# Kernel optimization log

Measured on AMD Instinct MI355X. Metric: run time of the kernel, lower is better.

## Reference

```python
import jax, jax.numpy as jnp
import numpy as np

N_NODES = 200000
N_EDGES = 500000
N_RELS = 256
D = 256  # rnn_in_dim == rnn_hid_dim


def setup_inputs() -> dict:
    key = jax.random.key(0)
    ks = jax.random.split(key, 8)
    src_nid = jax.random.randint(ks[0], (N_EDGES,), 0, N_NODES, dtype=jnp.int32)
    dst_nid = jax.random.randint(ks[1], (N_EDGES,), 0, N_NODES, dtype=jnp.int32)
    rel = jax.random.randint(ks[2], (N_EDGES,), 0, N_RELS, dtype=jnp.int32)
    static_entity_emb = jax.random.normal(ks[3], (N_NODES, D), dtype=jnp.float32)
    dynamic_relation_emb = jax.random.normal(ks[4], (N_RELS, 1, D, 2), dtype=jnp.float32)
    s = 1.0 / np.sqrt(D)
    W_ih = jax.random.uniform(ks[5], (3 * D, D), jnp.float32, -s, s)
    W_hh = jax.random.uniform(ks[6], (3 * D, D), jnp.float32, -s, s)
    kb1, kb2 = jax.random.split(ks[7])
    b_ih = jax.random.uniform(kb1, (3 * D,), jnp.float32, -s, s)
    b_hh = jax.random.uniform(kb2, (3 * D,), jnp.float32, -s, s)
    return {"src_nid": src_nid, "dst_nid": dst_nid, "rel": rel,
            "static_entity_emb": static_entity_emb,
            "dynamic_relation_emb": dynamic_relation_emb,
            "W_ih": W_ih, "W_hh": W_hh, "b_ih": b_ih, "b_hh": b_hh}


def _segment_mean(x, ids, num_segments):
    # x: [E, D], ids: [E] -> [R, D] mean per relation (0 where empty, as scatter_mean)
    sums = jax.ops.segment_sum(x, ids, num_segments=num_segments)
    cnts = jax.ops.segment_sum(jnp.ones((ids.shape[0],), x.dtype), ids,
                               num_segments=num_segments)
    return sums / jnp.maximum(cnts, 1.0)[:, None]


def _gru_cell(x, h, W_ih, W_hh, b_ih, b_hh):
    # PyTorch GRU cell, single step. x,h: [R, H]
    gi = x @ W_ih.T + b_ih            # [R, 3H]
    gh = h @ W_hh.T + b_hh            # [R, 3H]
    i_r, i_z, i_n = jnp.split(gi, 3, axis=-1)
    h_r, h_z, h_n = jnp.split(gh, 3, axis=-1)
    r = jax.nn.sigmoid(i_r + h_r)
    z = jax.nn.sigmoid(i_z + h_z)
    n = jnp.tanh(i_n + r * h_n)
    return (1.0 - z) * n + z * h


def reference(src_nid, dst_nid, rel, static_entity_emb, dynamic_relation_emb,
              W_ih, W_hh, b_ih, b_hh):
    R = dynamic_relation_emb.shape[0]
    # gather node embeddings by edge endpoints, mean-reduce per relation
    src_avg = _segment_mean(static_entity_emb[src_nid], rel, R)  # [R, D]
    dst_avg = _segment_mean(static_entity_emb[dst_nid], rel, R)  # [R, D]
    h_src = dynamic_relation_emb[:, 0, :, 0]  # num_layers==1 -> [R, H]
    h_dst = dynamic_relation_emb[:, 0, :, 1]
    new_src = _gru_cell(src_avg, h_src, W_ih, W_hh, b_ih, b_hh)
    new_dst = _gru_cell(dst_avg, h_dst, W_ih, W_hh, b_ih, b_hh)
    # [R, num_layers=1, H, 2]
    return jnp.stack([new_src, new_dst], axis=-1)[:, None, :, :]
```

## Files before the change

kernel.cpp:

```cpp
#include <hip/hip_runtime.h>
#include <math.h>

#define D 256
#define R 256
#define DIMC 64

__device__ __forceinline__ float sigmoidf(float x) {
    return 1.0f / (1.0f + expf(-x));
}

__global__ void zero_ws(float* ws, int n) {
    int i = blockIdx.x * blockDim.x + threadIdx.x;
    if (i < n) ws[i] = 0.0f;
}

__global__ __launch_bounds__(256) void hist_kernel(const int* __restrict__ rel,
                                                   int E,
                                                   float* __restrict__ counts) {
    __shared__ int h[R];
    h[threadIdx.x] = 0;
    __syncthreads();
    for (int e = blockIdx.x * blockDim.x + threadIdx.x; e < E;
         e += gridDim.x * blockDim.x)
        atomicAdd(&h[rel[e]], 1);
    __syncthreads();
    atomicAdd(&counts[threadIdx.x], (float)h[threadIdx.x]);
}

__global__ __launch_bounds__(1024, 8) void scatter_kernel(
    const int* __restrict__ src_nid, const int* __restrict__ dst_nid,
    const int* __restrict__ rel, const float* __restrict__ emb,
    float* __restrict__ src_sum, float* __restrict__ dst_sum, int E, int epb) {
    __shared__ float acc[R * DIMC];
    const int tid = threadIdx.x;
    for (int i = tid; i < R * DIMC; i += 1024) acc[i] = 0.0f;
    __syncthreads();

    const int* nids = blockIdx.z ? dst_nid : src_nid;
    float* gsum     = blockIdx.z ? dst_sum : src_sum;
    const int dimbase = blockIdx.y * DIMC;
    const int lane = tid & 63;
    const int wave = tid >> 6;
    const int start = blockIdx.x * epb;
    const int end   = (start + epb < E) ? (start + epb) : E;
    const int dl = dimbase + lane;

    for (int base = start + wave * 64; base < end; base += 1024) {
        int rem = end - base;
        int cnt = rem < 64 ? rem : 64;
        int mynid = 0, myrel = 0;
        if (lane < cnt) {
            mynid = nids[base + lane];
            myrel = rel[base + lane];
        }
        int i = 0;
        for (; i + 16 <= cnt; i += 16) {
            float v[16];
#pragma unroll
            for (int j = 0; j < 16; j++) {
                int n = __builtin_amdgcn_readlane(mynid, i + j);
                v[j] = emb[(size_t)n * D + dl];
            }
#pragma unroll
            for (int j = 0; j < 16; j++) {
                int rr = __builtin_amdgcn_readlane(myrel, i + j);
                atomicAdd(&acc[rr * DIMC + lane], v[j]);
            }
        }
        for (; i < cnt; i++) {
            int n  = __builtin_amdgcn_readlane(mynid, i);
            int rr = __builtin_amdgcn_readlane(myrel, i);
            float v = emb[(size_t)n * D + dl];
            atomicAdd(&acc[rr * DIMC + lane], v);
        }
    }
    __syncthreads();
    for (int i = tid; i < R * DIMC; i += 1024) {
        int r = i >> 6;
        int d = i & 63;
        atomicAdd(&gsum[r * D + dimbase + d], acc[i]);
    }
}

__global__ __launch_bounds__(256) void gru_kernel(
    const float* __restrict__ src_sum, const float* __restrict__ dst_sum,
    const float* __restrict__ counts, const float* __restrict__ dyn,
    const float* __restrict__ W_ih, const float* __restrict__ W_hh,
    const float* __restrict__ b_ih, const float* __restrict__ b_hh,
    float* __restrict__ out) {
    __shared__ float xs[D], xd[D], hs[D], hd[D];
    const int r = blockIdx.x, t = threadIdx.x;
    float inv = 1.0f / fmaxf(counts[r], 1.0f);
    xs[t] = src_sum[r * D + t] * inv;
    xd[t] = dst_sum[r * D + t] * inv;
    float h_s = dyn[(r * D + t) * 2 + 0];
    float h_d = dyn[(r * D + t) * 2 + 1];
    hs[t] = h_s;
    hd[t] = h_d;
    __syncthreads();

    float gis[3], gid[3], ghs[3], ghd[3];
#pragma unroll
    for (int g = 0; g < 3; g++) {
        int row = g * D + t;
        const float4* wi = (const float4*)(W_ih + (size_t)row * D);
        const float4* wh = (const float4*)(W_hh + (size_t)row * D);
        float ais = 0.f, aid = 0.f, ahs = 0.f, ahd = 0.f;
        for (int k = 0; k < D / 4; k++) {
            float4 a = wi[k];
            float4 b = wh[k];
            int k4 = k * 4;
            ais += a.x * xs[k4] + a.y * xs[k4 + 1] + a.z * xs[k4 + 2] + a.w * xs[k4 + 3];
            aid += a.x * xd[k4] + a.y * xd[k4 + 1] + a.z * xd[k4 + 2] + a.w * xd[k4 + 3];
            ahs += b.x * hs[k4] + b.y * hs[k4 + 1] + b.z * hs[k4 + 2] + b.w * hs[k4 + 3];
            ahd += b.x * hd[k4] + b.y * hd[k4 + 1] + b.z * hd[k4 + 2] + b.w * hd[k4 + 3];
        }
        float bi = b_ih[row];
        float bh = b_hh[row];
        gis[g] = ais + bi; gid[g] = aid + bi;
        ghs[g] = ahs + bh; ghd[g] = ahd + bh;
    }
    float rs = sigmoidf(gis[0] + ghs[0]);
    float zs = sigmoidf(gis[1] + ghs[1]);
    float ns = tanhf(gis[2] + rs * ghs[2]);
    float new_s = (1.0f - zs) * ns + zs * h_s;

    float rd = sigmoidf(gid[0] + ghd[0]);
    float zd = sigmoidf(gid[1] + ghd[1]);
    float nd = tanhf(gid[2] + rd * ghd[2]);
    float new_d = (1.0f - zd) * nd + zd * h_d;

    out[(r * D + t) * 2 + 0] = new_s;
    out[(r * D + t) * 2 + 1] = new_d;
}

extern "C" void kernel_launch(void* const* d_in, const int* in_sizes, int n_in,
                              void* d_out, int out_size, void* d_ws, size_t ws_size,
                              hipStream_t stream) {
    const int* src_nid = (const int*)d_in[0];
    const int* dst_nid = (const int*)d_in[1];
    const int* rel     = (const int*)d_in[2];
    const float* emb   = (const float*)d_in[3];
    const float* dyn   = (const float*)d_in[4];
    const float* W_ih  = (const float*)d_in[5];
    const float* W_hh  = (const float*)d_in[6];
    const float* b_ih  = (const float*)d_in[7];
    const float* b_hh  = (const float*)d_in[8];
    float* out = (float*)d_out;
    const int E = in_sizes[0];

    float* ws      = (float*)d_ws;
    float* src_sum = ws;
    float* dst_sum = ws + R * D;
    float* counts  = ws + 2 * R * D;
    const int nzero = 2 * R * D + R;

    zero_ws<<<(nzero + 255) / 256, 256, 0, stream>>>(ws, nzero);
    hist_kernel<<<256, 256, 0, stream>>>(rel, E, counts);

    const int chunks = 64;
    const int epb = (E + chunks - 1) / chunks;
    scatter_kernel<<<dim3(chunks, 4, 2), 1024, 0, stream>>>(
        src_nid, dst_nid, rel, emb, src_sum, dst_sum, E, epb);

    gru_kernel<<<R, 256, 0, stream>>>(src_sum, dst_sum, counts, dyn, W_ih, W_hh,
                                      b_ih, b_hh, out);
}
```

Before: 1.555 ms.

## Gather two edges per wave with float2 nontemporal loads in scatter kernel

The scatter kernel now splits each wave into two half-waves that handle different edges. Each lane loads a float2 of the embedding row with a nontemporal hint, so a wave gathers two edges' 64-dim slices per instruction instead of one. The shared accumulator layout is interleaved to match, and the final global atomics remap indices back to the right columns. The chunk count is halved and the launch-bounds occupancy hint is lowered, which gives fewer blocks, so fewer shared-to-global flush atomics but less parallelism.

```diff
diff --git a/kernel.cpp b/kernel.cpp
--- a/kernel.cpp
+++ b/kernel.cpp
@@ -3,7 +3,8 @@
 
 #define D 256
 #define R 256
-#define DIMC 64
+
+typedef float f2 __attribute__((ext_vector_type(2)));
 
 __device__ __forceinline__ float sigmoidf(float x) {
     return 1.0f / (1.0f + expf(-x));
@@ -27,23 +28,27 @@
     atomicAdd(&counts[threadIdx.x], (float)h[threadIdx.x]);
 }
 
-__global__ __launch_bounds__(1024, 8) void scatter_kernel(
+__global__ __launch_bounds__(1024, 4) void scatter_kernel(
     const int* __restrict__ src_nid, const int* __restrict__ dst_nid,
     const int* __restrict__ rel, const float* __restrict__ emb,
     float* __restrict__ src_sum, float* __restrict__ dst_sum, int E, int epb) {
-    __shared__ float acc[R * DIMC];
+    __shared__ float acc[R * 64];
     const int tid = threadIdx.x;
-    for (int i = tid; i < R * DIMC; i += 1024) acc[i] = 0.0f;
+    for (int i = tid; i < R * 64; i += 1024) acc[i] = 0.0f;
     __syncthreads();
 
     const int* nids = blockIdx.z ? dst_nid : src_nid;
     float* gsum     = blockIdx.z ? dst_sum : src_sum;
-    const int dimbase = blockIdx.y * DIMC;
+    const int dimbase = blockIdx.y * 64;
     const int lane = tid & 63;
     const int wave = tid >> 6;
+    const int half = lane >> 5;
+    const int m    = lane & 31;
     const int start = blockIdx.x * epb;
     const int end   = (start + epb < E) ? (start + epb) : E;
-    const int dl = dimbase + lane;
+
+    const f2* embv = (const f2*)emb;
+    const size_t rowoff = (size_t)(dimbase >> 1) + m;
 
     for (int base = start + wave * 64; base < end; base += 1024) {
         int rem = end - base;
@@ -53,32 +58,47 @@
             mynid = nids[base + lane];
             myrel = rel[base + lane];
         }
-        int i = 0;
-        for (; i + 16 <= cnt; i += 16) {
-            float v[16];
+        int steps = (cnt + 1) >> 1;
+        int j = 0;
+        for (; j + 16 <= steps; j += 16) {
+            int n[16], rr[16];
 #pragma unroll
-            for (int j = 0; j < 16; j++) {
-                int n = __builtin_amdgcn_readlane(mynid, i + j);
-                v[j] = emb[(size_t)n * D + dl];
+            for (int jj = 0; jj < 16; jj++) {
+                int e = 2 * (j + jj) + half;
+                n[jj]  = __shfl(mynid, e);
+                rr[jj] = __shfl(myrel, e);
             }
+            f2 v[16];
 #pragma unroll
-            for (int j = 0; j < 16; j++) {
-                int rr = __builtin_amdgcn_readlane(myrel, i + j);
-                atomicAdd(&acc[rr * DIMC + lane], v[j]);
+            for (int jj = 0; jj < 16; jj++)
+                v[jj] = __builtin_nontemporal_load(
+                    &embv[(size_t)n[jj] * 128 + rowoff]);
+#pragma unroll
+            for (int jj = 0; jj < 16; jj++) {
+                atomicAdd(&acc[rr[jj] * 64 + m],      v[jj].x);
+                atomicAdd(&acc[rr[jj] * 64 + 32 + m], v[jj].y);
             }
         }
-        for (; i < cnt; i++) {
-            int n  = __builtin_amdgcn_readlane(mynid, i);
-            int rr = __builtin_amdgcn_readlane(myrel, i);
-            float v = emb[(size_t)n * D + dl];
-            atomicAdd(&acc[rr * DIMC + lane], v);
+        for (; j < steps; j++) {
+            int e = 2 * j + half;
+            int valid = e < cnt;
+            int n  = valid ? __shfl(mynid, e) : 0;
+            int rr = __shfl(myrel, e);
+            f2 v = __builtin_nontemporal_load(&embv[(size_t)n * 128 + rowoff]);
+            if (valid) {
+                atomicAdd(&acc[rr * 64 + m],      v.x);
+                atomicAdd(&acc[rr * 64 + 32 + m], v.y);
+            }
         }
     }
     __syncthreads();
-    for (int i = tid; i < R * DIMC; i += 1024) {
-        int r = i >> 6;
-        int d = i & 63;
-        atomicAdd(&gsum[r * D + dimbase + d], acc[i]);
+    for (int i = tid; i < R * 64; i += 1024) {
+        int r  = i >> 6;
+        int rest = i & 63;
+        int k  = rest >> 5;
+        int mm = rest & 31;
+        int d  = dimbase + 2 * mm + k;
+        atomicAdd(&gsum[r * D + d], acc[i]);
     }
 }
 
@@ -158,7 +178,7 @@
     zero_ws<<<(nzero + 255) / 256, 256, 0, stream>>>(ws, nzero);
     hist_kernel<<<256, 256, 0, stream>>>(rel, E, counts);
 
-    const int chunks = 64;
+    const int chunks = 32;
     const int epb = (E + chunks - 1) / chunks;
     scatter_kernel<<<dim3(chunks, 4, 2), 1024, 0, stream>>>(
         src_nid, dst_nid, rel, emb, src_sum, dst_sum, E, epb);
```

Measured after the change: 1.612 ms. +3.6%, slower.

## Replace per-edge gather-scatter with node-sorted CSR accumulation of embeddings

Applied to the files above, without the earlier changes.

Builds a CSR of edge endpoints grouped by node (histogram, three-pass prefix scan, atomic-cursor fill of packed relation/side payloads). Each node embedding row is then read once and scattered into shared-memory per-relation accumulators for both the src and dst sides. This is meant to cut the random embedding gathers from one per endpoint to one per node, with rows read coalesced. In exchange it adds several preprocessing kernels and global atomics, and each node's payload loop runs serially within a half-wave, which can diverge.

```diff
diff --git a/kernel.cpp b/kernel.cpp
--- a/kernel.cpp
+++ b/kernel.cpp
@@ -3,20 +3,24 @@
 
 #define D 256
 #define R 256
-#define DIMC 64
+#define DIMC 32
+#define NODE_CHUNKS 64
 
 __device__ __forceinline__ float sigmoidf(float x) {
     return 1.0f / (1.0f + expf(-x));
 }
 
-__global__ void zero_ws(float* ws, int n) {
-    int i = blockIdx.x * blockDim.x + threadIdx.x;
-    if (i < n) ws[i] = 0.0f;
-}
-
-__global__ __launch_bounds__(256) void hist_kernel(const int* __restrict__ rel,
-                                                   int E,
-                                                   float* __restrict__ counts) {
+__global__ void zero_f(float* p, int n) {
+    int i = blockIdx.x * blockDim.x + threadIdx.x;
+    if (i < n) p[i] = 0.0f;
+}
+__global__ void zero_i(int* p, int n) {
+    int i = blockIdx.x * blockDim.x + threadIdx.x;
+    if (i < n) p[i] = 0;
+}
+
+__global__ __launch_bounds__(256) void hist_rel(const int* __restrict__ rel,
+                                                int E, float* __restrict__ counts) {
     __shared__ int h[R];
     h[threadIdx.x] = 0;
     __syncthreads();
@@ -27,58 +31,113 @@
     atomicAdd(&counts[threadIdx.x], (float)h[threadIdx.x]);
 }
 
-__global__ __launch_bounds__(1024, 8) void scatter_kernel(
-    const int* __restrict__ src_nid, const int* __restrict__ dst_nid,
-    const int* __restrict__ rel, const float* __restrict__ emb,
-    float* __restrict__ src_sum, float* __restrict__ dst_sum, int E, int epb) {
-    __shared__ float acc[R * DIMC];
+__global__ __launch_bounds__(256) void hist_nodes(const int* __restrict__ src,
+                                                  const int* __restrict__ dst,
+                                                  int E, int* __restrict__ cnt) {
+    int i = blockIdx.x * blockDim.x + threadIdx.x;
+    if (i < 2 * E) {
+        int n = (i < E) ? src[i] : dst[i - E];
+        atomicAdd(&cnt[n], 1);
+    }
+}
+
+__global__ __launch_bounds__(1024) void scan1(const int* __restrict__ cnt, int N,
+                                              int* __restrict__ offs,
+                                              int* __restrict__ bsum) {
+    __shared__ int s[1024];
+    int t = threadIdx.x, i = blockIdx.x * 1024 + t;
+    int x = (i < N) ? cnt[i] : 0;
+    s[t] = x;
+    __syncthreads();
+    for (int o = 1; o < 1024; o <<= 1) {
+        int v = (t >= o) ? s[t - o] : 0;
+        __syncthreads();
+        s[t] += v;
+        __syncthreads();
+    }
+    if (i < N) offs[i] = s[t] - x;
+    if (t == 1023) bsum[blockIdx.x] = s[t];
+}
+__global__ __launch_bounds__(1024) void scan2(const int* __restrict__ bsum, int NB,
+                                              int* __restrict__ bexcl) {
+    __shared__ int s[1024];
+    int t = threadIdx.x;
+    int x = (t < NB) ? bsum[t] : 0;
+    s[t] = x;
+    __syncthreads();
+    for (int o = 1; o < 1024; o <<= 1) {
+        int v = (t >= o) ? s[t - o] : 0;
+        __syncthreads();
+        s[t] += v;
+        __syncthreads();
+    }
+    if (t < NB) bexcl[t] = s[t] - x;
+}
+__global__ __launch_bounds__(1024) void scan3(int* __restrict__ offs, int N,
+                                              const int* __restrict__ bexcl,
+                                              int total) {
+    int t = threadIdx.x, i = blockIdx.x * 1024 + t;
+    if (i < N) offs[i] += bexcl[blockIdx.x];
+    if (i == 0) offs[N] = total;
+}
+
+__global__ __launch_bounds__(256) void build_pay(const int* __restrict__ src,
+                                                 const int* __restrict__ dst,
+                                                 const int* __restrict__ rel, int E,
+                                                 const int* __restrict__ offs,
+                                                 int* __restrict__ cursor,
+                                                 unsigned short* __restrict__ pay) {
+    int i = blockIdx.x * blockDim.x + threadIdx.x;
+    if (i >= 2 * E) return;
+    int side = (i >= E) ? 1 : 0;
+    int e = side ? i - E : i;
+    int n = side ? dst[e] : src[e];
+    int r = rel[e];
+    int pos = offs[n] + atomicAdd(&cursor[n], 1);
+    pay[pos] = (unsigned short)(r | (side << 8));
+}
+
+__global__ __launch_bounds__(256) void node_accum(const float* __restrict__ emb,
+                                                  const int* __restrict__ offs,
+                                                  const unsigned short* __restrict__ pay,
+                                                  float* __restrict__ src_sum,
+                                                  float* __restrict__ dst_sum,
+                                                  int N, int npb) {
+    __shared__ float acc[2 * R * DIMC];
     const int tid = threadIdx.x;
-    for (int i = tid; i < R * DIMC; i += 1024) acc[i] = 0.0f;
-    __syncthreads();
-
-    const int* nids = blockIdx.z ? dst_nid : src_nid;
-    float* gsum     = blockIdx.z ? dst_sum : src_sum;
+    for (int i = tid; i < 2 * R * DIMC; i += 256) acc[i] = 0.0f;
+    __syncthreads();
+
     const int dimbase = blockIdx.y * DIMC;
-    const int lane = tid & 63;
-    const int wave = tid >> 6;
-    const int start = blockIdx.x * epb;
-    const int end   = (start + epb < E) ? (start + epb) : E;
-    const int dl = dimbase + lane;
-
-    for (int base = start + wave * 64; base < end; base += 1024) {
-        int rem = end - base;
-        int cnt = rem < 64 ? rem : 64;
-        int mynid = 0, myrel = 0;
-        if (lane < cnt) {
-            mynid = nids[base + lane];
-            myrel = rel[base + lane];
-        }
-        int i = 0;
-        for (; i + 16 <= cnt; i += 16) {
-            float v[16];
-#pragma unroll
-            for (int j = 0; j < 16; j++) {
-                int n = __builtin_amdgcn_readlane(mynid, i + j);
-                v[j] = emb[(size_t)n * D + dl];
-            }
-#pragma unroll
-            for (int j = 0; j < 16; j++) {
-                int rr = __builtin_amdgcn_readlane(myrel, i + j);
-                atomicAdd(&acc[rr * DIMC + lane], v[j]);
+    const int wave = tid >> 6, lane = tid & 63;
+    const int half = lane >> 5, m = lane & 31;
+    const int n0 = blockIdx.x * npb;
+    const int n1 = (n0 + npb < N) ? (n0 + npb) : N;
+
+    int n = n0 + wave * 2;
+    float v = 0.0f;
+    if (n + half < n1) v = emb[(size_t)(n + half) * D + dimbase + m];
+    for (; n < n1; n += 8) {
+        int nA = n + half;
+        float vnext = 0.0f;
+        int nn = n + 8 + half;
+        if (nn < n1) vnext = emb[(size_t)nn * D + dimbase + m];
+        if (nA < n1) {
+            int oA = offs[nA];
+            int cA = offs[nA + 1] - oA;
+            for (int k = 0; k < cA; k++) {
+                int p = pay[oA + k];
+                int r = p & 255, side = p >> 8;
+                atomicAdd(&acc[(side << 13) + (r << 5) + m], v);
             }
         }
-        for (; i < cnt; i++) {
-            int n  = __builtin_amdgcn_readlane(mynid, i);
-            int rr = __builtin_amdgcn_readlane(myrel, i);
-            float v = emb[(size_t)n * D + dl];
-            atomicAdd(&acc[rr * DIMC + lane], v);
-        }
-    }
-    __syncthreads();
-    for (int i = tid; i < R * DIMC; i += 1024) {
-        int r = i >> 6;
-        int d = i & 63;
-        atomicAdd(&gsum[r * D + dimbase + d], acc[i]);
+        v = vnext;
+    }
+    __syncthreads();
+    for (int i = tid; i < 2 * R * DIMC; i += 256) {
+        int side = i >> 13, r = (i >> 5) & 255, mm = i & 31;
+        float* g = side ? dst_sum : src_sum;
+        atomicAdd(&g[r * D + dimbase + mm], acc[i]);
     }
 }
 
@@ -148,21 +207,34 @@
     const float* b_hh  = (const float*)d_in[8];
     float* out = (float*)d_out;
     const int E = in_sizes[0];
+    const int N = in_sizes[3] / D;
 
     float* ws      = (float*)d_ws;
     float* src_sum = ws;
     float* dst_sum = ws + R * D;
     float* counts  = ws + 2 * R * D;
-    const int nzero = 2 * R * D + R;
-
-    zero_ws<<<(nzero + 255) / 256, 256, 0, stream>>>(ws, nzero);
-    hist_kernel<<<256, 256, 0, stream>>>(rel, E, counts);
-
-    const int chunks = 64;
-    const int epb = (E + chunks - 1) / chunks;
-    scatter_kernel<<<dim3(chunks, 4, 2), 1024, 0, stream>>>(
-        src_nid, dst_nid, rel, emb, src_sum, dst_sum, E, epb);
-
+    const int nzf  = 2 * R * D + R;
+    int* cnt    = (int*)(ws + nzf);
+    int* cursor = cnt + N;
+    int* offs   = cursor + N;
+    int* bsum   = offs + N + 1;
+    int* bexcl  = bsum + 1024;
+    unsigned short* pay = (unsigned short*)(bexcl + 1024);
+
+    const int NB  = (N + 1023) / 1024;
+    const int npb = (N + NODE_CHUNKS - 1) / NODE_CHUNKS;
+
+    zero_f<<<(nzf + 255) / 256, 256, 0, stream>>>(ws, nzf);
+    zero_i<<<(2 * N + 255) / 256, 256, 0, stream>>>(cnt, 2 * N);
+    hist_rel<<<256, 256, 0, stream>>>(rel, E, counts);
+    hist_nodes<<<(2 * E + 255) / 256, 256, 0, stream>>>(src_nid, dst_nid, E, cnt);
+    scan1<<<NB, 1024, 0, stream>>>(cnt, N, offs, bsum);
+    scan2<<<1, 1024, 0, stream>>>(bsum, NB, bexcl);
+    scan3<<<NB, 1024, 0, stream>>>(offs, N, bexcl, 2 * E);
+    build_pay<<<(2 * E + 255) / 256, 256, 0, stream>>>(src_nid, dst_nid, rel, E,
+                                                       offs, cursor, pay);
+    node_accum<<<dim3(NODE_CHUNKS, D / DIMC), 256, 0, stream>>>(
+        emb, offs, pay, src_sum, dst_sum, N, npb);
     gru_kernel<<<R, 256, 0, stream>>>(src_sum, dst_sum, counts, dyn, W_ih, W_hh,
                                       b_ih, b_hh, out);
 }
```

New measurement: 1.688 ms. 1.09x slower.
